# Kernel tuning notes

Hardware: AMD Instinct MI355X
Metric: run time of the kernel (lower is better)

Reference implementation:

```python
import jax, jax.numpy as jnp
import numpy as np

RH, RW = 4, 4

def window_sum(x, rh, rw):
    # cumsum along H (axis 2)
    cum_h = jnp.cumsum(x, axis=2)
    wh = 2 * rh + 1
    top = cum_h[:, :, rh:wh, :]
    midh = cum_h[:, :, wh:, :] - cum_h[:, :, :-wh, :]
    bot = cum_h[:, :, -1:, :] - cum_h[:, :, -wh:-rh - 1, :]
    out = jnp.concatenate([top, midh, bot], axis=2)
    # cumsum along W (axis 3)
    cum_w = jnp.cumsum(out, axis=3)
    ww = 2 * rw + 1
    left = cum_w[:, :, :, rw:ww]
    midw = cum_w[:, :, :, ww:] - cum_w[:, :, :, :-ww]
    right = cum_w[:, :, :, -1:] - cum_w[:, :, :, -ww:-rw - 1]
    return jnp.concatenate([left, midw, right], axis=3)


def setup_inputs() -> dict:
    key = jax.random.key(0)
    x = jax.random.normal(key, (16, 3, 1024, 1024), dtype=jnp.float32)
    return {"x": x}


def reference(x):
    win_sum = window_sum(x, RH, RW)
    count = window_sum(jnp.ones_like(x), RH, RW)
    return win_sum / count
```

## Files before the change

kernel.cpp:

```cpp
#include <hip/hip_runtime.h>

#define HH 1024
#define WW 1024
#define BH 64
#define RAD 4

__global__ __launch_bounds__(256) void box_kernel(const float* __restrict__ x,
                                                  float* __restrict__ out) {
    __shared__ __align__(16) float hring[9][WW];

    const int tid = threadIdx.x;
    const int img = blockIdx.y;
    const int r0  = blockIdx.x * BH;
    const int c   = tid * 4;

    const float* xin = x + (size_t)img * HH * WW;
    float*       o   = out + (size_t)img * HH * WW;

    float inv_cw[4];
#pragma unroll
    for (int j = 0; j < 4; ++j) {
        int cc = c + j;
        int lo = cc - RAD < 0 ? 0 : cc - RAD;
        int hi = cc + RAD > WW - 1 ? WW - 1 : cc + RAD;
        inv_cw[j] = 1.0f / (float)(hi - lo + 1);
    }

    const bool first = (tid == 0);
    const bool last  = (tid == 255);

    float vs0 = 0.f, vs1 = 0.f, vs2 = 0.f, vs3 = 0.f;

#pragma unroll 1
    for (int k = 0; k < 9; ++k) {
        int rr = r0 - 5 + k;
        float4 a, b, d;
        if (rr >= 0) {
            const float* row = xin + (size_t)rr * WW;
            b = *(const float4*)(row + c);
            a = first ? make_float4(0.f,0.f,0.f,0.f) : *(const float4*)(row + c - 4);
            d = last  ? make_float4(0.f,0.f,0.f,0.f) : *(const float4*)(row + c + 4);
        } else {
            a = b = d = make_float4(0.f,0.f,0.f,0.f);
        }
        float h0 = ((a.x + a.y) + (a.z + a.w)) + ((b.x + b.y) + (b.z + b.w)) + d.x;
        float h1 = h0 - a.x + d.y;
        float h2 = h1 - a.y + d.z;
        float h3 = h2 - a.z + d.w;
        *(float4*)&hring[k][c] = make_float4(h0, h1, h2, h3);
        vs0 += h0; vs1 += h1; vs2 += h2; vs3 += h3;
    }

    int slot = 0;
#pragma unroll 2
    for (int r = r0; r < r0 + BH; ++r) {
        int rl = r + RAD;
        float4 a, b, d;
        if (rl < HH) {
            const float* row = xin + (size_t)rl * WW;
            b = *(const float4*)(row + c);
            a = first ? make_float4(0.f,0.f,0.f,0.f) : *(const float4*)(row + c - 4);
            d = last  ? make_float4(0.f,0.f,0.f,0.f) : *(const float4*)(row + c + 4);
        } else {
            a = b = d = make_float4(0.f,0.f,0.f,0.f);
        }
        float h0 = ((a.x + a.y) + (a.z + a.w)) + ((b.x + b.y) + (b.z + b.w)) + d.x;
        float h1 = h0 - a.x + d.y;
        float h2 = h1 - a.y + d.z;
        float h3 = h2 - a.z + d.w;

        float4 hold = *(const float4*)&hring[slot][c];
        vs0 += h0 - hold.x;
        vs1 += h1 - hold.y;
        vs2 += h2 - hold.z;
        vs3 += h3 - hold.w;
        *(float4*)&hring[slot][c] = make_float4(h0, h1, h2, h3);
        slot = (slot == 8) ? 0 : slot + 1;

        int lo = r - RAD < 0 ? 0 : r - RAD;
        int hi = r + RAD > HH - 1 ? HH - 1 : r + RAD;
        float inv_ch = 1.0f / (float)(hi - lo + 1);

        float4 o4 = make_float4(vs0 * inv_ch * inv_cw[0],
                                vs1 * inv_ch * inv_cw[1],
                                vs2 * inv_ch * inv_cw[2],
                                vs3 * inv_ch * inv_cw[3]);
        *(float4*)(o + (size_t)r * WW + c) = o4;
    }
}

extern "C" void kernel_launch(void* const* d_in, const int* in_sizes, int n_in,
                              void* d_out, int out_size, void* d_ws, size_t ws_size,
                              hipStream_t stream) {
    const float* x = (const float*)d_in[0];
    float* out = (float*)d_out;
    int n_images = in_sizes[0] / (HH * WW);
    dim3 grid(HH / BH, n_images);
    dim3 block(256);
    box_kernel<<<grid, block, 0, stream>>>(x, out);
}
```

Measured before the change: 346.1 us.

## Move row ring to registers, halve strip height, add interior fast path and swizzle

The sliding ring of horizontal sums moves from a 36KB shared-memory array into per-thread registers, unrolled by 9 so slot indices are static. Strip height drops from 64 to 32 rows, which doubles the block count but also the halo reads per strip. Interior strips get a fast path with a constant 1/9 vertical weight and pointer increments, and outputs use nontemporal stores. Block IDs are remapped with an XCD-style swizzle, and launch bounds ask for 4 blocks per CU.

```diff
diff --git a/kernel.cpp b/kernel.cpp
--- a/kernel.cpp
+++ b/kernel.cpp
@@ -2,90 +2,124 @@
 
 #define HH 1024
 #define WW 1024
-#define BH 64
+#define BH 32
 #define RAD 4
+#define NSTRIP (HH / BH)
 
-__global__ __launch_bounds__(256) void box_kernel(const float* __restrict__ x,
-                                                  float* __restrict__ out) {
-    __shared__ __align__(16) float hring[9][WW];
+typedef float vfloat4 __attribute__((ext_vector_type(4)));
 
+struct HS { float h0, h1, h2, h3; };
+
+__device__ __forceinline__ HS hsum_row(const float* __restrict__ row, int c,
+                                       bool first, bool last) {
+    float4 b = *(const float4*)(row + c);
+    float4 a, d;
+    if (first) a = make_float4(0.f, 0.f, 0.f, 0.f);
+    else       a = *(const float4*)(row + c - 4);
+    if (last)  d = make_float4(0.f, 0.f, 0.f, 0.f);
+    else       d = *(const float4*)(row + c + 4);
+    HS h;
+    h.h0 = ((a.x + a.y) + (a.z + a.w)) + ((b.x + b.y) + (b.z + b.w)) + d.x;
+    h.h1 = h.h0 - a.x + d.y;
+    h.h2 = h.h1 - a.y + d.z;
+    h.h3 = h.h2 - a.z + d.w;
+    return h;
+}
+
+#define STEP_FAST(J) do {                                                  \
+    HS h = hsum_row(rowp, c, first, last);                                 \
+    vs0 += h.h0 - ring[J].h0;                                              \
+    vs1 += h.h1 - ring[J].h1;                                              \
+    vs2 += h.h2 - ring[J].h2;                                              \
+    vs3 += h.h3 - ring[J].h3;                                              \
+    ring[J] = h;                                                           \
+    vfloat4 o4 = {vs0 * w0, vs1 * w1, vs2 * w2, vs3 * w3};                 \
+    __builtin_nontemporal_store(o4, (vfloat4*)(op + c));                   \
+    rowp += WW; op += WW;                                                  \
+} while (0)
+
+#define STEP_GEN(J) do {                                                   \
+    int rl = r + RAD;                                                      \
+    HS h;                                                                  \
+    if (rl < HH) h = hsum_row(xin + (size_t)rl * WW, c, first, last);      \
+    else { h.h0 = 0.f; h.h1 = 0.f; h.h2 = 0.f; h.h3 = 0.f; }               \
+    vs0 += h.h0 - ring[J].h0;                                              \
+    vs1 += h.h1 - ring[J].h1;                                              \
+    vs2 += h.h2 - ring[J].h2;                                              \
+    vs3 += h.h3 - ring[J].h3;                                              \
+    ring[J] = h;                                                           \
+    int lo = r - RAD; if (lo < 0) lo = 0;                                  \
+    int hi = r + RAD; if (hi > HH - 1) hi = HH - 1;                        \
+    float ich = 1.0f / (float)(hi - lo + 1);                               \
+    vfloat4 o4 = {vs0 * ich * sw[0], vs1 * ich * sw[1],                    \
+                  vs2 * ich * sw[2], vs3 * ich * sw[3]};                   \
+    __builtin_nontemporal_store(o4, (vfloat4*)(o + (size_t)r * WW + c));   \
+    ++r;                                                                   \
+} while (0)
+
+__global__ __launch_bounds__(256, 4)
+void box_kernel(const float* __restrict__ x, float* __restrict__ out) {
     const int tid = threadIdx.x;
-    const int img = blockIdx.y;
-    const int r0  = blockIdx.x * BH;
-    const int c   = tid * 4;
 
-    const float* xin = x + (size_t)img * HH * WW;
-    float*       o   = out + (size_t)img * HH * WW;
+    const int lin  = blockIdx.x + NSTRIP * blockIdx.y;
+    const int nblk = NSTRIP * gridDim.y;
+    const int cpx  = nblk >> 3;
+    const int swz  = (lin & 7) * cpx + (lin >> 3);
+    const int strip = swz & (NSTRIP - 1);
+    const int img   = swz / NSTRIP;
 
-    float inv_cw[4];
+    const int r0 = strip * BH;
+    const int c  = tid * 4;
+    const bool first = (tid == 0);
+    const bool last  = (tid == 255);
+
+    const float* __restrict__ xin = x + (size_t)img * (HH * WW);
+    float* __restrict__ o = out + (size_t)img * (HH * WW);
+
+    float sw[4];
 #pragma unroll
     for (int j = 0; j < 4; ++j) {
         int cc = c + j;
         int lo = cc - RAD < 0 ? 0 : cc - RAD;
         int hi = cc + RAD > WW - 1 ? WW - 1 : cc + RAD;
-        inv_cw[j] = 1.0f / (float)(hi - lo + 1);
+        sw[j] = 1.0f / (float)(hi - lo + 1);
     }
 
-    const bool first = (tid == 0);
-    const bool last  = (tid == 255);
-
+    HS ring[9];
     float vs0 = 0.f, vs1 = 0.f, vs2 = 0.f, vs3 = 0.f;
-
-#pragma unroll 1
+#pragma unroll
     for (int k = 0; k < 9; ++k) {
-        int rr = r0 - 5 + k;
-        float4 a, b, d;
-        if (rr >= 0) {
-            const float* row = xin + (size_t)rr * WW;
-            b = *(const float4*)(row + c);
-            a = first ? make_float4(0.f,0.f,0.f,0.f) : *(const float4*)(row + c - 4);
-            d = last  ? make_float4(0.f,0.f,0.f,0.f) : *(const float4*)(row + c + 4);
-        } else {
-            a = b = d = make_float4(0.f,0.f,0.f,0.f);
-        }
-        float h0 = ((a.x + a.y) + (a.z + a.w)) + ((b.x + b.y) + (b.z + b.w)) + d.x;
-        float h1 = h0 - a.x + d.y;
-        float h2 = h1 - a.y + d.z;
-        float h3 = h2 - a.z + d.w;
-        *(float4*)&hring[k][c] = make_float4(h0, h1, h2, h3);
-        vs0 += h0; vs1 += h1; vs2 += h2; vs3 += h3;
+        int rr = r0 - RAD - 1 + k;
+        HS h;
+        if (rr >= 0) h = hsum_row(xin + (size_t)rr * WW, c, first, last);
+        else { h.h0 = 0.f; h.h1 = 0.f; h.h2 = 0.f; h.h3 = 0.f; }
+        ring[k] = h;
+        vs0 += h.h0; vs1 += h.h1; vs2 += h.h2; vs3 += h.h3;
     }
 
-    int slot = 0;
-#pragma unroll 2
-    for (int r = r0; r < r0 + BH; ++r) {
-        int rl = r + RAD;
-        float4 a, b, d;
-        if (rl < HH) {
-            const float* row = xin + (size_t)rl * WW;
-            b = *(const float4*)(row + c);
-            a = first ? make_float4(0.f,0.f,0.f,0.f) : *(const float4*)(row + c - 4);
-            d = last  ? make_float4(0.f,0.f,0.f,0.f) : *(const float4*)(row + c + 4);
-        } else {
-            a = b = d = make_float4(0.f,0.f,0.f,0.f);
+    const bool interior = (r0 >= RAD) && (r0 + BH + RAD <= HH);
+
+    if (interior) {
+        const float w0 = sw[0] * (1.0f / 9.0f);
+        const float w1 = sw[1] * (1.0f / 9.0f);
+        const float w2 = sw[2] * (1.0f / 9.0f);
+        const float w3 = sw[3] * (1.0f / 9.0f);
+        const float* __restrict__ rowp = xin + (size_t)(r0 + RAD) * WW;
+        float* __restrict__ op = o + (size_t)r0 * WW;
+#pragma unroll 1
+        for (int chunk = 0; chunk < 3; ++chunk) {
+            STEP_FAST(0); STEP_FAST(1); STEP_FAST(2); STEP_FAST(3); STEP_FAST(4);
+            STEP_FAST(5); STEP_FAST(6); STEP_FAST(7); STEP_FAST(8);
         }
-        float h0 = ((a.x + a.y) + (a.z + a.w)) + ((b.x + b.y) + (b.z + b.w)) + d.x;
-        float h1 = h0 - a.x + d.y;
-        float h2 = h1 - a.y + d.z;
-        float h3 = h2 - a.z + d.w;
-
-        float4 hold = *(const float4*)&hring[slot][c];
-        vs0 += h0 - hold.x;
-        vs1 += h1 - hold.y;
-        vs2 += h2 - hold.z;
-        vs3 += h3 - hold.w;
-        *(float4*)&hring[slot][c] = make_float4(h0, h1, h2, h3);
-        slot = (slot == 8) ? 0 : slot + 1;
-
-        int lo = r - RAD < 0 ? 0 : r - RAD;
-        int hi = r + RAD > HH - 1 ? HH - 1 : r + RAD;
-        float inv_ch = 1.0f / (float)(hi - lo + 1);
-
-        float4 o4 = make_float4(vs0 * inv_ch * inv_cw[0],
-                                vs1 * inv_ch * inv_cw[1],
-                                vs2 * inv_ch * inv_cw[2],
-                                vs3 * inv_ch * inv_cw[3]);
-        *(float4*)(o + (size_t)r * WW + c) = o4;
+        STEP_FAST(0); STEP_FAST(1); STEP_FAST(2); STEP_FAST(3); STEP_FAST(4);
+    } else {
+        int r = r0;
+#pragma unroll 1
+        for (int chunk = 0; chunk < 3; ++chunk) {
+            STEP_GEN(0); STEP_GEN(1); STEP_GEN(2); STEP_GEN(3); STEP_GEN(4);
+            STEP_GEN(5); STEP_GEN(6); STEP_GEN(7); STEP_GEN(8);
+        }
+        STEP_GEN(0); STEP_GEN(1); STEP_GEN(2); STEP_GEN(3); STEP_GEN(4);
     }
 }
 
@@ -95,7 +129,7 @@
     const float* x = (const float*)d_in[0];
     float* out = (float*)d_out;
     int n_images = in_sizes[0] / (HH * WW);
-    dim3 grid(HH / BH, n_images);
+    dim3 grid(NSTRIP, n_images);
     dim3 block(256);
     box_kernel<<<grid, block, 0, stream>>>(x, out);
 }
```

After: 366.5 us. 5.9% more time.
